# Kernel optimization log

Hardware: AMD Instinct MI355X
Metric: run time of the kernel (lower is better)

Reference implementation:

```python
import jax, jax.numpy as jnp
import numpy as np

B, N, C = 8, 4096, 768
H, HD = 12, 64          # num_heads, head_dim = C // H
M = HD * 2              # rand_feat_dim
LAM = 0.3
NUM_STEP = 5


def setup_inputs() -> dict:
    key = jax.random.key(0)
    k1, k2, k3, k4 = jax.random.split(key, 4)
    x = jax.random.normal(k1, (B, N, C), dtype=jnp.float32)
    Wqkv = jax.random.normal(k2, (C, 2 * C), dtype=jnp.float32) * 0.02
    Wproj = jax.random.normal(k3, (C, C), dtype=jnp.float32) * 0.02
    bproj = jnp.zeros((C,), dtype=jnp.float32)
    rand_matrix = jax.random.normal(k4, (H, HD, M), dtype=jnp.float32)
    return {"x": x, "Wqkv": Wqkv, "Wproj": Wproj, "bproj": bproj,
            "rand_matrix": rand_matrix}


def _soft(z, t):
    # sign(z) * relu(|z| - t): soft-thresholding (ISTA proximal step)
    return jnp.sign(z) * jax.nn.relu(jnp.abs(z) - t)


def reference(x, Wqkv, Wproj, bproj, rand_matrix):
    Bn, Nn, Cn = x.shape
    Hh, hd, m = rand_matrix.shape
    scale = hd ** (-0.5)

    qkv = x @ Wqkv                                   # [B,N,2C]
    q = qkv[..., :Cn].reshape(Bn, Nn, Hh, hd).transpose(0, 2, 1, 3)  # [B,H,N,hd]
    v = qkv[..., Cn:].reshape(Bn, Nn, Hh, hd).transpose(0, 2, 1, 3)  # [B,H,N,hd]

    # random-feature map: exp(q @ proj - ||q||^2 / 2) / sqrt(m)
    qs = q * scale ** 0.5
    rf = jnp.exp(jnp.einsum('bhnd,hdm->bhnm', qs, rand_matrix)
                 - 0.5 * jnp.sum(qs * qs, axis=-1, keepdims=True)) / m ** 0.5
    # F.normalize(p=2, dim=-2): normalize over the sequence axis
    qn = rf / jnp.maximum(jnp.linalg.norm(rf, axis=-2, keepdims=True), 1e-12)

    kk = jnp.einsum('bhnm,bhnp->bhmp', qn, qn)       # [B,H,m,m]
    kv = jnp.einsum('bhnm,bhnd->bhmd', qn, v)        # [B,H,m,hd]

    # Lipschitz bound: max row L1 norm of kk, detached
    L = jax.lax.stop_gradient(
        jnp.max(jnp.sum(jnp.abs(kk), axis=-1), axis=-1))[..., None, None] + 1.0

    # unrolled ISTA soft-thresholding loop
    s = _soft(kv, LAM)
    for _ in range(NUM_STEP):
        s = _soft(s - (kk @ s - kv) / L, LAM / L)

    out = jnp.einsum('bhnm,bhmd->bhnd', qn, s)       # [B,H,N,hd]
    out = out.transpose(0, 2, 1, 3).reshape(Bn, Nn, Cn)
    return out @ Wproj + bproj
```

## Files before the change

kernel.cpp:

```cpp
#include <hip/hip_runtime.h>


typedef __attribute__((ext_vector_type(8))) short bf16x8;
typedef __attribute__((ext_vector_type(4))) float f32x4;

#define GLD16(gptr, lptr)                                                              \
  __builtin_amdgcn_global_load_lds((const __attribute__((address_space(1))) void*)(gptr), \
                                   (__attribute__((address_space(3))) void*)(lptr), 16, 0, 0)

__device__ __forceinline__ unsigned short f2bf(float f) {
  union { float f; unsigned int u; } v; v.f = f;
  unsigned int r = v.u + 0x7fffu + ((v.u >> 16) & 1u);
  return (unsigned short)(r >> 16);
}
__device__ __forceinline__ float bf2f(unsigned short s) {
  union { unsigned int u; float f; } v; v.u = ((unsigned int)s) << 16;
  return v.f;
}
__device__ __forceinline__ float rn_of(float css) {
  return 1.f / fmaxf(sqrtf(css), 1e-12f);
}

template<int BM, int BN>
__device__ __forceinline__ void gemm_core_nt(
    const unsigned short* __restrict__ A, int lda,
    const unsigned short* __restrict__ B0,
    const unsigned short* __restrict__ B1, int brows0, int ldb,
    int K,
    f32x4 (&acc)[BM / 32][BN / 32],
    unsigned short* As, unsigned short* Bs) {
  constexpr int MT = BM / 32, NT = BN / 32;
  const int tid = threadIdx.x;
  const int lane = tid & 63, wave = tid >> 6;
  const int wm = (wave >> 1) * (BM / 2), wn = (wave & 1) * (BN / 2);
  const int l16 = lane & 15, quad = lane >> 4;
  const int arow = tid >> 2;
  const int akos = (((tid & 3) ^ ((arow >> 1) & 3)) << 3);
  const int fsw = (l16 >> 1) & 3;
#pragma unroll
  for (int i = 0; i < MT; i++)
#pragma unroll
    for (int j = 0; j < NT; j++)
#pragma unroll
      for (int r = 0; r < 4; r++) acc[i][j][r] = 0.f;

  for (int k0 = 0; k0 < K; k0 += 32) {
    __syncthreads();
#pragma unroll
    for (int c = 0; c < BM / 64; c++) {
      const unsigned short* gp = A + (long)(arow + c * 64) * lda + k0 + akos;
      GLD16(gp, As + (c * 256 + wave * 64) * 8);
    }
#pragma unroll
    for (int c = 0; c < BN / 64; c++) {
      int row = arow + c * 64;
      const unsigned short* bp = (row < brows0) ? (B0 + (long)row * ldb)
                                                : (B1 + (long)(row - brows0) * ldb);
      GLD16(bp + k0 + akos, Bs + (c * 256 + wave * 64) * 8);
    }
    __syncthreads();
    bf16x8 af[MT], bfr[NT];
#pragma unroll
    for (int i = 0; i < MT; i++)
      af[i] = *(const bf16x8*)(As + (wm + i * 16 + l16) * 32 + ((quad ^ fsw) * 8));
#pragma unroll
    for (int j = 0; j < NT; j++)
      bfr[j] = *(const bf16x8*)(Bs + (wn + j * 16 + l16) * 32 + ((quad ^ fsw) * 8));
#pragma unroll
    for (int i = 0; i < MT; i++)
#pragma unroll
      for (int j = 0; j < NT; j++)
        acc[i][j] = __builtin_amdgcn_mfma_f32_16x16x32_bf16(af[i], bfr[j], acc[i][j], 0, 0, 0);
  }
}

__global__ __launch_bounds__(256) void k_convert_bf16(const float* __restrict__ in,
                                                      unsigned short* __restrict__ out, long n4) {
  long i = (long)blockIdx.x * 256 + threadIdx.x;
  if (i < n4) {
    float4 v = ((const float4*)in)[i];
    unsigned short o[4] = {f2bf(v.x), f2bf(v.y), f2bf(v.z), f2bf(v.w)};
    ((uint2*)out)[i] = *(uint2*)o;
  }
}

__global__ __launch_bounds__(256) void k_transpose_tiled(const float* __restrict__ in,
                                                         unsigned short* __restrict__ out,
                                                         int R, int C, float scale) {
  __shared__ float t[32][33];
  const float* ib = in + (long)blockIdx.z * R * C;
  unsigned short* ob = out + (long)blockIdx.z * R * C;
  int c0 = blockIdx.x * 32, r0 = blockIdx.y * 32;
  int tx = threadIdx.x & 31, ty = threadIdx.x >> 5;
#pragma unroll
  for (int k = 0; k < 32; k += 8)
    t[ty + k][tx] = ib[(long)(r0 + ty + k) * C + c0 + tx];
  __syncthreads();
#pragma unroll
  for (int k = 0; k < 32; k += 8)
    ob[(long)(c0 + ty + k) * R + r0 + tx] = f2bf(t[tx][ty + k] * scale);
}

__global__ __launch_bounds__(256) void k_gemm_qkv(const unsigned short* __restrict__ xbf,
                                                  const unsigned short* __restrict__ wqkvT,
                                                  unsigned short* __restrict__ q,
                                                  unsigned short* __restrict__ vT) {
  __shared__ __align__(16) unsigned short pool[8576];
  unsigned short* As = pool;
  unsigned short* Bs = pool + 4096;
  f32x4 acc[4][4];
  const int L = blockIdx.x;
  const int xcd = L & 7, slot = L >> 3;
  const int rt = xcd * 32 + slot / 12;
  const int ct = slot % 12;
  const int tid = threadIdx.x, lane = tid & 63, wave = tid >> 6;
  const int l16 = lane & 15, quad = lane >> 4;
  const int wm = (wave >> 1) * 64, wn = (wave & 1) * 64;

  const unsigned short* A = xbf + (long)rt * 128 * 768;
  const unsigned short* B = wqkvT + (long)ct * 128 * 768;
  gemm_core_nt<128, 128>(A, 768, B, B, 128, 768, 768, acc, As, Bs);

  const int b = rt >> 5;
  const int nbase = (rt & 31) * 128;
  if (ct < 6) {
#pragma unroll
    for (int i = 0; i < 4; i++)
#pragma unroll
      for (int j = 0; j < 4; j++)
#pragma unroll
        for (int r = 0; r < 4; r++) {
          int col = ct * 128 + wn + j * 16 + l16;
          int h = col >> 6, d = col & 63;
          int n = nbase + wm + i * 16 + quad * 4 + r;
          q[((long)(b * 12 + h) * 4096 + n) * 64 + d] = f2bf(acc[i][j][r]);
        }
  } else {
    for (int hh = 0; hh < 2; hh++) {
      __syncthreads();
      if ((wave >> 1) == hh) {
#pragma unroll
        for (int i = 0; i < 4; i++)
#pragma unroll
          for (int j = 0; j < 4; j++)
#pragma unroll
            for (int r = 0; r < 4; r++)
              pool[(i * 16 + quad * 4 + r) * 134 + wn + j * 16 + l16] = f2bf(acc[i][j][r]);
      }
      __syncthreads();
#pragma unroll
      for (int c = 0; c < 4; c++) {
        int chunk = tid + c * 256;
        int col = chunk >> 3, nj = (chunk & 7) * 8;
        unsigned short o[8];
#pragma unroll
        for (int e = 0; e < 8; e++) o[e] = pool[(nj + e) * 134 + col];
        int vcol = ct * 128 - 768 + col;
        int h = vcol >> 6, d = vcol & 63;
        long n = nbase + hh * 64 + nj;
        *(uint4*)&vT[((long)(b * 12 + h) * 64 + d) * 4096 + n] = *(uint4*)o;
      }
    }
  }
}

__global__ __launch_bounds__(256) void k_gemm_rf(const unsigned short* __restrict__ q,
                                                 const unsigned short* __restrict__ rmT,
                                                 unsigned short* __restrict__ qnT,
                                                 float* __restrict__ colss) {
  __shared__ __align__(16) unsigned short smem[16384];
  __shared__ float hnp[256];
  __shared__ float css[128];
  unsigned short* Asm = smem;
  unsigned short* Bsm = smem + 8192;
  unsigned short* pool = smem;
  f32x4 acc[4][4];
  const int nt = blockIdx.x, bh = blockIdx.y, h = bh % 12;
  const int tid = threadIdx.x, lane = tid & 63, wave = tid >> 6;
  const int l16 = lane & 15, quad = lane >> 4;
  const int wm = (wave >> 1) * 64, wn = (wave & 1) * 64;
  const int fsw = (l16 >> 1) & 3;
  const unsigned short* Aq = q + ((long)bh * 4096 + nt * 128) * 64;
  const unsigned short* Brm = rmT + (long)h * 8192;

#pragma unroll
  for (int c = 0; c < 4; c++) {
    int chunk = c * 256 + tid;
    int row = chunk >> 3, ko8 = chunk & 7;
    int kc = ko8 >> 2;
    int c2s = (ko8 & 3) ^ ((row >> 1) & 3);
    *(uint4*)(Asm + kc * 4096 + row * 32 + c2s * 8) = *(const uint4*)(Aq + (long)row * 64 + ko8 * 8);
    *(uint4*)(Bsm + kc * 4096 + row * 32 + c2s * 8) = *(const uint4*)(Brm + (long)row * 64 + ko8 * 8);
  }
  for (int i = tid; i < 128; i += 256) css[i] = 0.f;
  __syncthreads();
  {
    const unsigned short* ap = Asm + (tid & 1) * 4096 + (tid >> 1) * 32;
    float ssum = 0.f;
#pragma unroll
    for (int e = 0; e < 32; e++) { float f = bf2f(ap[e]); ssum += f * f; }
    hnp[tid] = ssum;
  }
#pragma unroll
  for (int i = 0; i < 4; i++)
#pragma unroll
    for (int j = 0; j < 4; j++)
#pragma unroll
      for (int r = 0; r < 4; r++) acc[i][j][r] = 0.f;
#pragma unroll
  for (int kc = 0; kc < 2; kc++) {
    bf16x8 af[4], bfr[4];
#pragma unroll
    for (int i = 0; i < 4; i++)
      af[i] = *(const bf16x8*)(Asm + kc * 4096 + (wm + i * 16 + l16) * 32 + ((quad ^ fsw) * 8));
#pragma unroll
    for (int j = 0; j < 4; j++)
      bfr[j] = *(const bf16x8*)(Bsm + kc * 4096 + (wn + j * 16 + l16) * 32 + ((quad ^ fsw) * 8));
#pragma unroll
    for (int i = 0; i < 4; i++)
#pragma unroll
      for (int j = 0; j < 4; j++)
        acc[i][j] = __builtin_amdgcn_mfma_f32_16x16x32_bf16(af[i], bfr[j], acc[i][j], 0, 0, 0);
  }
  __syncthreads();
  float hnv[4][4];
#pragma unroll
  for (int i = 0; i < 4; i++)
#pragma unroll
    for (int r = 0; r < 4; r++) {
      int row = wm + i * 16 + quad * 4 + r;
      hnv[i][r] = 0.0625f * (hnp[2 * row] + hnp[2 * row + 1]);
    }
#pragma unroll
  for (int j = 0; j < 4; j++) {
    int col = wn + j * 16 + l16;
    float cp = 0.f;
#pragma unroll
    for (int i = 0; i < 4; i++)
#pragma unroll
      for (int r = 0; r < 4; r++) {
        float v = __expf(acc[i][j][r] - hnv[i][r]) * 0.08838834764831845f;
        acc[i][j][r] = v;
        cp += v * v;
      }
    atomicAdd(&css[col], cp);
  }
  __syncthreads();
  for (int i = tid; i < 128; i += 256) atomicAdd(&colss[bh * 128 + i], css[i]);
  for (int hh = 0; hh < 2; hh++) {
    __syncthreads();
    if ((wave >> 1) == hh) {
#pragma unroll
      for (int i = 0; i < 4; i++)
#pragma unroll
        for (int j = 0; j < 4; j++)
#pragma unroll
          for (int r = 0; r < 4; r++)
            pool[(i * 16 + quad * 4 + r) * 134 + wn + j * 16 + l16] = f2bf(acc[i][j][r]);
    }
    __syncthreads();
#pragma unroll
    for (int c = 0; c < 4; c++) {
      int chunk = tid + c * 256;
      int m = chunk >> 3, nj = (chunk & 7) * 8;
      unsigned short o[8];
#pragma unroll
      for (int e = 0; e < 8; e++) o[e] = pool[(nj + e) * 134 + m];
      *(uint4*)&qnT[((long)bh * 128 + m) * 4096 + nt * 128 + hh * 64 + nj] = *(uint4*)o;
    }
  }
}

__global__ __launch_bounds__(256) void k_gemm_kkkv(const unsigned short* __restrict__ qnT,
                                                   const unsigned short* __restrict__ vT,
                                                   const float* __restrict__ colss,
                                                   unsigned short* __restrict__ kkp) {
  __shared__ __align__(16) unsigned short As[128 * 32], Bs[192 * 32];
  f32x4 acc[4][6];
  const int ks = blockIdx.x, bh = blockIdx.y;
  const unsigned short* A = qnT + (long)bh * 128 * 4096 + ks * 512;
  const unsigned short* B1 = vT + (long)bh * 64 * 4096 + ks * 512;
  gemm_core_nt<128, 192>(A, 4096, A, B1, 128, 4096, 512, acc, As, Bs);
  const int lane = threadIdx.x & 63, wave = threadIdx.x >> 6;
  const int l16 = lane & 15, quad = lane >> 4;
  const int wm = (wave >> 1) * 64, wn = (wave & 1) * 96;
  unsigned short* dst = kkp + ((long)ks * 96 + bh) * 24576;
  float rnr[4][4];
#pragma unroll
  for (int i = 0; i < 4; i++)
#pragma unroll
    for (int r = 0; r < 4; r++)
      rnr[i][r] = rn_of(colss[bh * 128 + wm + i * 16 + quad * 4 + r]);
#pragma unroll
  for (int j = 0; j < 6; j++) {
    int col = wn + j * 16 + l16;
    float rnc = (col < 128) ? rn_of(colss[bh * 128 + col]) : 1.f;
#pragma unroll
    for (int i = 0; i < 4; i++)
#pragma unroll
      for (int r = 0; r < 4; r++) {
        int row = wm + i * 16 + quad * 4 + r;
        dst[row * 192 + col] = f2bf(acc[i][j][r] * rnr[i][r] * rnc);
      }
  }
}

__global__ __launch_bounds__(256) void k_ista(const unsigned short* __restrict__ kkp,
                                              const float* __restrict__ colss,
                                              unsigned short* __restrict__ sT) {
  __shared__ __align__(16) unsigned short kks[128 * 144];
  __shared__ __align__(16) unsigned short ssT[64 * 144];
  __shared__ float kvs[128 * 64];
  __shared__ float red[128];
  __shared__ float rns[128];
  const int tid = threadIdx.x, lane = tid & 63, wave = tid >> 6;
  const int l16 = lane & 15, quad = lane >> 4;
  const int wm = (wave >> 1) * 64, wn = (wave & 1) * 32;
  const int bh = blockIdx.x;
  const unsigned short* base = kkp + (long)bh * 24576;
  for (int idx = tid; idx < 3072; idx += 256) {
    int m = idx / 24, c8 = idx % 24;
    float f[8] = {0.f, 0.f, 0.f, 0.f, 0.f, 0.f, 0.f, 0.f};
#pragma unroll
    for (int ks = 0; ks < 8; ks++) {
      union { uint4 u; unsigned short s[8]; } u;
      u.u = *(const uint4*)(base + (long)ks * 2359296 + m * 192 + c8 * 8);
#pragma unroll
      for (int e = 0; e < 8; e++) f[e] += bf2f(u.s[e]);
    }
    if (c8 < 16) {
#pragma unroll
      for (int e = 0; e < 8; e++) kks[m * 144 + c8 * 8 + e] = f2bf(f[e]);
    } else {
#pragma unroll
      for (int e = 0; e < 8; e++) kvs[m * 64 + (c8 - 16) * 8 + e] = f[e];
    }
  }
  __syncthreads();
  float kv[4][2][4];
#pragma unroll
  for (int i = 0; i < 4; i++)
#pragma unroll
    for (int j = 0; j < 2; j++)
#pragma unroll
      for (int r = 0; r < 4; r++) {
        int m = wm + i * 16 + quad * 4 + r, d = wn + j * 16 + l16;
        kv[i][j][r] = kvs[m * 64 + d];
      }
  if (tid < 128) {
    float rs = 0.f;
    const unsigned short* rp = kks + tid * 144;
    for (int p = 0; p < 128; p++) rs += fabsf(bf2f(rp[p]));
    red[tid] = rs;
    rns[tid] = rn_of(colss[bh * 128 + tid]);
  }
  __syncthreads();
  for (int o = 64; o > 0; o >>= 1) {
    if (tid < o) red[tid] = fmaxf(red[tid], red[tid + o]);
    __syncthreads();
  }
  const float L = red[0] + 1.f;
  const float invL = 1.f / L;
  const float lamL = 0.3f * invL;
  float sreg[4][2][4];
#pragma unroll
  for (int i = 0; i < 4; i++)
#pragma unroll
    for (int j = 0; j < 2; j++)
#pragma unroll
      for (int r = 0; r < 4; r++) {
        float z = kv[i][j][r];
        float az = fabsf(z) - 0.3f;
        float s = az > 0.f ? copysignf(az, z) : 0.f;
        sreg[i][j][r] = s;
        ssT[(wn + j * 16 + l16) * 144 + wm + i * 16 + quad * 4 + r] = f2bf(s);
      }
  for (int step = 0; step < 5; step++) {
    __syncthreads();
    f32x4 acc[4][2];
#pragma unroll
    for (int i = 0; i < 4; i++)
#pragma unroll
      for (int j = 0; j < 2; j++)
#pragma unroll
        for (int r = 0; r < 4; r++) acc[i][j][r] = 0.f;
#pragma unroll
    for (int kc = 0; kc < 4; kc++) {
      bf16x8 af[4], bfj[2];
#pragma unroll
      for (int i = 0; i < 4; i++)
        af[i] = *(const bf16x8*)(kks + (wm + i * 16 + l16) * 144 + kc * 32 + quad * 8);
#pragma unroll
      for (int j = 0; j < 2; j++)
        bfj[j] = *(const bf16x8*)(ssT + (wn + j * 16 + l16) * 144 + kc * 32 + quad * 8);
#pragma unroll
      for (int i = 0; i < 4; i++)
#pragma unroll
        for (int j = 0; j < 2; j++)
          acc[i][j] = __builtin_amdgcn_mfma_f32_16x16x32_bf16(af[i], bfj[j], acc[i][j], 0, 0, 0);
    }
    __syncthreads();
#pragma unroll
    for (int i = 0; i < 4; i++)
#pragma unroll
      for (int j = 0; j < 2; j++)
#pragma unroll
        for (int r = 0; r < 4; r++) {
          float z = sreg[i][j][r] - (acc[i][j][r] - kv[i][j][r]) * invL;
          float az = fabsf(z) - lamL;
          float s = az > 0.f ? copysignf(az, z) : 0.f;
          sreg[i][j][r] = s;
          ssT[(wn + j * 16 + l16) * 144 + wm + i * 16 + quad * 4 + r] = f2bf(s);
        }
  }
#pragma unroll
  for (int i = 0; i < 4; i++)
#pragma unroll
    for (int j = 0; j < 2; j++)
#pragma unroll
      for (int r = 0; r < 4; r++) {
        int m = wm + i * 16 + quad * 4 + r, d = wn + j * 16 + l16;
        sT[(long)bh * 8192 + d * 128 + m] = f2bf(sreg[i][j][r] * rns[m]);
      }
}

__global__ __launch_bounds__(256) void k_gemm_attn(const unsigned short* __restrict__ qnT,
                                                   const unsigned short* __restrict__ sT,
                                                   unsigned short* __restrict__ attn) {
  __shared__ __align__(16) unsigned short As2[32 * 128];
  __shared__ __align__(16) unsigned short Bs[64 * 32];
  f32x4 acc[4][2];
  const int nt = blockIdx.x, bh = blockIdx.y;
  const int b = bh / 12, h = bh % 12;
  const int tid = threadIdx.x, lane = tid & 63, wave = tid >> 6;
  const int l16 = lane & 15, quad = lane >> 4;
  const int wm = (wave >> 1) * 64, wn = (wave & 1) * 32;
  const int fsw = (l16 >> 1) & 3;
#pragma unroll
  for (int i = 0; i < 4; i++)
#pragma unroll
    for (int j = 0; j < 2; j++)
#pragma unroll
      for (int r = 0; r < 4; r++) acc[i][j][r] = 0.f;
  for (int k0 = 0; k0 < 128; k0 += 32) {
    __syncthreads();
#pragma unroll
    for (int c = 0; c < 2; c++) {
      int chunk = tid + c * 256;
      int kr = chunk >> 4, n0 = (chunk & 15) * 8;
      const unsigned short* gp = qnT + ((long)bh * 128 + k0 + kr) * 4096 + nt * 128 + n0;
      GLD16(gp, As2 + (c * 256 + wave * 64) * 8);
    }
    {
      int dd = tid >> 2;
      int ko = (((tid & 3) ^ ((dd >> 1) & 3)) * 8);
      const unsigned short* gp = sT + ((long)bh * 64 + dd) * 128 + k0 + ko;
      GLD16(gp, Bs + wave * 512);
    }
    __syncthreads();
    bf16x8 af[4], bfr[2];
#pragma unroll
    for (int i = 0; i < 4; i++) {
      union { bf16x8 v; unsigned short s[8]; } u;
#pragma unroll
      for (int e = 0; e < 8; e++) u.s[e] = As2[(quad * 8 + e) * 128 + wm + i * 16 + l16];
      af[i] = u.v;
    }
#pragma unroll
    for (int j = 0; j < 2; j++)
      bfr[j] = *(const bf16x8*)&Bs[(wn + j * 16 + l16) * 32 + ((quad ^ fsw) * 8)];
#pragma unroll
    for (int i = 0; i < 4; i++)
#pragma unroll
      for (int j = 0; j < 2; j++)
        acc[i][j] = __builtin_amdgcn_mfma_f32_16x16x32_bf16(af[i], bfr[j], acc[i][j], 0, 0, 0);
  }
#pragma unroll
  for (int i = 0; i < 4; i++)
#pragma unroll
    for (int j = 0; j < 2; j++)
#pragma unroll
      for (int r = 0; r < 4; r++) {
        int n = nt * 128 + wm + i * 16 + quad * 4 + r;
        int dd = wn + j * 16 + l16;
        attn[((long)b * 4096 + n) * 768 + h * 64 + dd] = f2bf(acc[i][j][r]);
      }
}

__global__ __launch_bounds__(256) void k_gemm_proj(const unsigned short* __restrict__ attn,
                                                   const unsigned short* __restrict__ wprojT,
                                                   const float* __restrict__ bias,
                                                   float* __restrict__ out) {
  __shared__ __align__(16) unsigned short As[128 * 32], Bs[128 * 32];
  f32x4 acc[4][4];
  const int Lb = blockIdx.x;
  const int xcd = Lb & 7, slot = Lb >> 3;
  const int rt = xcd * 32 + slot / 6;
  const int ct = slot % 6;
  const unsigned short* A = attn + (long)rt * 128 * 768;
  const unsigned short* B = wprojT + (long)ct * 128 * 768;
  gemm_core_nt<128, 128>(A, 768, B, B, 128, 768, 768, acc, As, Bs);
  const int lane = threadIdx.x & 63, wave = threadIdx.x >> 6;
  const int l16 = lane & 15, quad = lane >> 4;
  const int wm = (wave >> 1) * 64, wn = (wave & 1) * 64;
  long row0 = (long)rt * 128, col0 = (long)ct * 128;
#pragma unroll
  for (int i = 0; i < 4; i++)
#pragma unroll
    for (int j = 0; j < 4; j++) {
      int col = (int)col0 + wn + j * 16 + l16;
      float bv = bias[col];
#pragma unroll
      for (int r = 0; r < 4; r++) {
        long row = row0 + wm + i * 16 + quad * 4 + r;
        out[row * 768 + col] = acc[i][j][r] + bv;
      }
    }
}

extern "C" void kernel_launch(void* const* d_in, const int* in_sizes, int n_in,
                              void* d_out, int out_size, void* d_ws, size_t ws_size,
                              hipStream_t stream) {
  const float* x = (const float*)d_in[0];
  const float* Wqkv = (const float*)d_in[1];
  const float* Wproj = (const float*)d_in[2];
  const float* bproj = (const float*)d_in[3];
  const float* rm = (const float*)d_in[4];
  float* out = (float*)d_out;

  size_t o = 0;
  char* wsb = (char*)d_ws;
  auto take = [&](size_t b) { char* p = wsb + o; o += b; return p; };
  unsigned short* wqkvT = (unsigned short*)take(2359296);
  unsigned short* wprojT = (unsigned short*)take(1179648);
  unsigned short* rmT = (unsigned short*)take(196608);
  unsigned short* q = (unsigned short*)take(50331648);
  unsigned short* vT = (unsigned short*)take(50331648);
  float* colss = (float*)take(49152);
  unsigned short* sT = (unsigned short*)take(1572864);
  if (ws_size < o) return;

  unsigned short* xbf = (unsigned short*)d_out;
  unsigned short* qnT = (unsigned short*)d_out;
  unsigned short* kkp = q;
  unsigned short* attnbf = q;

  hipMemsetAsync(colss, 0, 49152, stream);

  k_convert_bf16<<<24576, 256, 0, stream>>>(x, xbf, 6291456L);
  k_transpose_tiled<<<dim3(48, 24, 1), 256, 0, stream>>>(Wqkv, wqkvT, 768, 1536, 1.0f);
  k_transpose_tiled<<<dim3(24, 24, 1), 256, 0, stream>>>(Wproj, wprojT, 768, 768, 1.0f);
  k_transpose_tiled<<<dim3(4, 2, 12), 256, 0, stream>>>(rm, rmT, 64, 128, 0.3535533905932738f);
  k_gemm_qkv<<<3072, 256, 0, stream>>>(xbf, wqkvT, q, vT);
  k_gemm_rf<<<dim3(32, 96), 256, 0, stream>>>(q, rmT, qnT, colss);
  k_gemm_kkkv<<<dim3(8, 96), 256, 0, stream>>>(qnT, vT, colss, kkp);
  k_ista<<<96, 256, 0, stream>>>(kkp, colss, sT);
  k_gemm_attn<<<dim3(32, 96), 256, 0, stream>>>(qnT, sT, attnbf);
  k_gemm_proj<<<1536, 256, 0, stream>>>(attnbf, wprojT, bproj, out);
}
```

Measured before the change: 471.5 us.

## Use 256x256 tiled 8-wave GEMM core for QKV and projection GEMMs

Adds a new GEMM core with 256x256 block tiles, 512 threads, double-buffered direct-to-LDS loads, and MFMA work split into two halves around the prefetch, with priority hints. The QKV and output-projection GEMMs move to this core with larger tiles and fewer blocks, aiming for better operand reuse and overlap of loads with MFMA. The V transpose epilogue is rewritten to read contiguous LDS rows. The trade-off is more registers and LDS per block and fewer blocks, which lowers occupancy and can leave the tail poorly balanced.

```diff
diff --git a/kernel.cpp b/kernel.cpp
--- a/kernel.cpp
+++ b/kernel.cpp
@@ -19,6 +19,90 @@
 }
 __device__ __forceinline__ float rn_of(float css) {
   return 1.f / fmaxf(sqrtf(css), 1e-12f);
+}
+
+template<int KT>
+__device__ __forceinline__ void gemm256_core(
+    const unsigned short* __restrict__ A,
+    const unsigned short* __restrict__ B,
+    int ldk,
+    f32x4 (&acc)[8][4],
+    unsigned short* smem) {
+  const int tid = threadIdx.x;
+  const int lane = tid & 63, wave = tid >> 6;
+  const int l16 = lane & 15, quad = lane >> 4;
+  const int wr = wave >> 2, wc = wave & 3;
+  const int fsw = (l16 >> 1) & 3;
+  const int r0 = tid >> 2;
+  const int gsw = (((tid & 3) ^ ((r0 >> 1) & 3)) << 3);
+
+#pragma unroll
+  for (int i = 0; i < 8; i++)
+#pragma unroll
+    for (int j = 0; j < 4; j++)
+#pragma unroll
+      for (int r = 0; r < 4; r++) acc[i][j][r] = 0.f;
+
+  const unsigned short* Ag0 = A + (long)r0 * ldk + gsw;
+  const unsigned short* Ag1 = A + (long)(r0 + 128) * ldk + gsw;
+  const unsigned short* Bg0 = B + (long)r0 * ldk + gsw;
+  const unsigned short* Bg1 = B + (long)(r0 + 128) * ldk + gsw;
+  const int ldsW = wave * 64 * 8;
+
+  auto stage = [&](int t, int b) {
+    unsigned short* Ab = smem + b * 16384;
+    unsigned short* Bb = Ab + 8192;
+    const int k0 = t * 32;
+    GLD16(Ag0 + k0, Ab + ldsW);
+    GLD16(Ag1 + k0, Ab + 4096 + ldsW);
+    GLD16(Bg0 + k0, Bb + ldsW);
+    GLD16(Bg1 + k0, Bb + 4096 + ldsW);
+  };
+
+  stage(0, 0);
+  stage(1, 1);
+  asm volatile("s_waitcnt vmcnt(4)" ::: "memory");
+  __builtin_amdgcn_s_barrier();
+
+  for (int t = 0; t < KT; t++) {
+    const int b = t & 1;
+    const unsigned short* Ab = smem + b * 16384;
+    const unsigned short* Bb = Ab + 8192;
+    bf16x8 af[8], bf[4];
+#pragma unroll
+    for (int i = 0; i < 8; i++)
+      af[i] = *(const bf16x8*)(Ab + (wr * 128 + i * 16 + l16) * 32 + ((quad ^ fsw) * 8));
+#pragma unroll
+    for (int j = 0; j < 4; j++)
+      bf[j] = *(const bf16x8*)(Bb + (wc * 64 + j * 16 + l16) * 32 + ((quad ^ fsw) * 8));
+    asm volatile("s_waitcnt lgkmcnt(0)" ::: "memory");
+    __builtin_amdgcn_s_barrier();
+    __builtin_amdgcn_s_setprio(1);
+#pragma unroll
+    for (int i = 0; i < 8; i++)
+#pragma unroll
+      for (int j = 0; j < 2; j++)
+        acc[i][j] = __builtin_amdgcn_mfma_f32_16x16x32_bf16(af[i], bf[j], acc[i][j], 0, 0, 0);
+    __builtin_amdgcn_s_setprio(0);
+    asm volatile("" ::: "memory");
+    __builtin_amdgcn_s_barrier();
+    if (t + 2 < KT) stage(t + 2, b);
+    asm volatile("" ::: "memory");
+    __builtin_amdgcn_s_barrier();
+    __builtin_amdgcn_s_setprio(1);
+#pragma unroll
+    for (int i = 0; i < 8; i++)
+#pragma unroll
+      for (int j = 2; j < 4; j++)
+        acc[i][j] = __builtin_amdgcn_mfma_f32_16x16x32_bf16(af[i], bf[j], acc[i][j], 0, 0, 0);
+    __builtin_amdgcn_s_setprio(0);
+    if (t + 2 < KT) {
+      asm volatile("s_waitcnt vmcnt(4)" ::: "memory");
+    } else {
+      asm volatile("s_waitcnt vmcnt(0)" ::: "memory");
+    }
+    __builtin_amdgcn_s_barrier();
+  }
 }
 
 template<int BM, int BN>
@@ -101,64 +185,59 @@
     ob[(long)(c0 + ty + k) * R + r0 + tx] = f2bf(t[tx][ty + k] * scale);
 }
 
-__global__ __launch_bounds__(256) void k_gemm_qkv(const unsigned short* __restrict__ xbf,
-                                                  const unsigned short* __restrict__ wqkvT,
-                                                  unsigned short* __restrict__ q,
-                                                  unsigned short* __restrict__ vT) {
-  __shared__ __align__(16) unsigned short pool[8576];
-  unsigned short* As = pool;
-  unsigned short* Bs = pool + 4096;
-  f32x4 acc[4][4];
+__global__ __launch_bounds__(512, 2) void k_gemm_qkv256(const unsigned short* __restrict__ xbf,
+                                                        const unsigned short* __restrict__ wqkvT,
+                                                        unsigned short* __restrict__ q,
+                                                        unsigned short* __restrict__ vT) {
+  __shared__ __align__(16) unsigned short smem[36864];
+  f32x4 acc[8][4];
   const int L = blockIdx.x;
   const int xcd = L & 7, slot = L >> 3;
-  const int rt = xcd * 32 + slot / 12;
-  const int ct = slot % 12;
+  const int rt = xcd * 16 + slot / 6;
+  const int ct = slot % 6;
+  gemm256_core<24>(xbf + (long)rt * 256 * 768, wqkvT + (long)ct * 256 * 768, 768, acc, smem);
+
   const int tid = threadIdx.x, lane = tid & 63, wave = tid >> 6;
   const int l16 = lane & 15, quad = lane >> 4;
-  const int wm = (wave >> 1) * 64, wn = (wave & 1) * 64;
-
-  const unsigned short* A = xbf + (long)rt * 128 * 768;
-  const unsigned short* B = wqkvT + (long)ct * 128 * 768;
-  gemm_core_nt<128, 128>(A, 768, B, B, 128, 768, 768, acc, As, Bs);
-
-  const int b = rt >> 5;
-  const int nbase = (rt & 31) * 128;
-  if (ct < 6) {
-#pragma unroll
-    for (int i = 0; i < 4; i++)
-#pragma unroll
-      for (int j = 0; j < 4; j++)
+  const int wr = wave >> 2, wc = wave & 3;
+  const int b = rt >> 4;
+  const int nbase = (rt & 15) * 256;
+  if (ct < 3) {
+#pragma unroll
+    for (int i = 0; i < 8; i++)
+#pragma unroll
+      for (int j = 0; j < 4; j++) {
+        int col = ct * 256 + wc * 64 + j * 16 + l16;
+        int h = col >> 6, d = col & 63;
 #pragma unroll
         for (int r = 0; r < 4; r++) {
-          int col = ct * 128 + wn + j * 16 + l16;
-          int h = col >> 6, d = col & 63;
-          int n = nbase + wm + i * 16 + quad * 4 + r;
+          int n = nbase + wr * 128 + i * 16 + quad * 4 + r;
           q[((long)(b * 12 + h) * 4096 + n) * 64 + d] = f2bf(acc[i][j][r]);
         }
+      }
   } else {
+    unsigned short* pool = smem;
     for (int hh = 0; hh < 2; hh++) {
       __syncthreads();
-      if ((wave >> 1) == hh) {
-#pragma unroll
-        for (int i = 0; i < 4; i++)
+      if (wr == hh) {
+#pragma unroll
+        for (int i = 0; i < 8; i++)
 #pragma unroll
           for (int j = 0; j < 4; j++)
 #pragma unroll
             for (int r = 0; r < 4; r++)
-              pool[(i * 16 + quad * 4 + r) * 134 + wn + j * 16 + l16] = f2bf(acc[i][j][r]);
+              pool[(wc * 64 + j * 16 + l16) * 136 + i * 16 + quad * 4 + r] = f2bf(acc[i][j][r]);
       }
       __syncthreads();
 #pragma unroll
-      for (int c = 0; c < 4; c++) {
-        int chunk = tid + c * 256;
-        int col = chunk >> 3, nj = (chunk & 7) * 8;
-        unsigned short o[8];
-#pragma unroll
-        for (int e = 0; e < 8; e++) o[e] = pool[(nj + e) * 134 + col];
-        int vcol = ct * 128 - 768 + col;
+      for (int it = 0; it < 8; it++) {
+        int chunk = it * 512 + tid;
+        int col = chunk >> 4, ng = chunk & 15;
+        uint4 val = *(const uint4*)&pool[col * 136 + ng * 8];
+        int vcol = (ct - 3) * 256 + col;
         int h = vcol >> 6, d = vcol & 63;
-        long n = nbase + hh * 64 + nj;
-        *(uint4*)&vT[((long)(b * 12 + h) * 64 + d) * 4096 + n] = *(uint4*)o;
+        long n = nbase + hh * 128 + ng * 8;
+        *(uint4*)&vT[((long)(b * 12 + h) * 64 + d) * 4096 + n] = val;
       }
     }
   }
@@ -487,32 +566,30 @@
       }
 }
 
-__global__ __launch_bounds__(256) void k_gemm_proj(const unsigned short* __restrict__ attn,
-                                                   const unsigned short* __restrict__ wprojT,
-                                                   const float* __restrict__ bias,
-                                                   float* __restrict__ out) {
-  __shared__ __align__(16) unsigned short As[128 * 32], Bs[128 * 32];
-  f32x4 acc[4][4];
-  const int Lb = blockIdx.x;
-  const int xcd = Lb & 7, slot = Lb >> 3;
-  const int rt = xcd * 32 + slot / 6;
-  const int ct = slot % 6;
-  const unsigned short* A = attn + (long)rt * 128 * 768;
-  const unsigned short* B = wprojT + (long)ct * 128 * 768;
-  gemm_core_nt<128, 128>(A, 768, B, B, 128, 768, 768, acc, As, Bs);
-  const int lane = threadIdx.x & 63, wave = threadIdx.x >> 6;
-  const int l16 = lane & 15, quad = lane >> 4;
-  const int wm = (wave >> 1) * 64, wn = (wave & 1) * 64;
-  long row0 = (long)rt * 128, col0 = (long)ct * 128;
-#pragma unroll
-  for (int i = 0; i < 4; i++)
+__global__ __launch_bounds__(512, 2) void k_gemm_proj256(const unsigned short* __restrict__ attn,
+                                                         const unsigned short* __restrict__ wprojT,
+                                                         const float* __restrict__ bias,
+                                                         float* __restrict__ out) {
+  __shared__ __align__(16) unsigned short smem[32768];
+  f32x4 acc[8][4];
+  const int L = blockIdx.x;
+  const int xcd = L & 7, slot = L >> 3;
+  const int rt = xcd * 16 + slot / 3;
+  const int ct = slot % 3;
+  gemm256_core<24>(attn + (long)rt * 256 * 768, wprojT + (long)ct * 256 * 768, 768, acc, smem);
+  const int tid = threadIdx.x, lane = tid & 63, wave = tid >> 6;
+  const int l16 = lane & 15, quad = lane >> 4;
+  const int wr = wave >> 2, wc = wave & 3;
+  const long row0 = (long)rt * 256 + wr * 128;
+#pragma unroll
+  for (int i = 0; i < 8; i++)
 #pragma unroll
     for (int j = 0; j < 4; j++) {
-      int col = (int)col0 + wn + j * 16 + l16;
+      int col = ct * 256 + wc * 64 + j * 16 + l16;
       float bv = bias[col];
 #pragma unroll
       for (int r = 0; r < 4; r++) {
-        long row = row0 + wm + i * 16 + quad * 4 + r;
+        long row = row0 + i * 16 + quad * 4 + r;
         out[row * 768 + col] = acc[i][j][r] + bv;
       }
     }
@@ -551,10 +628,10 @@
   k_transpose_tiled<<<dim3(48, 24, 1), 256, 0, stream>>>(Wqkv, wqkvT, 768, 1536, 1.0f);
   k_transpose_tiled<<<dim3(24, 24, 1), 256, 0, stream>>>(Wproj, wprojT, 768, 768, 1.0f);
   k_transpose_tiled<<<dim3(4, 2, 12), 256, 0, stream>>>(rm, rmT, 64, 128, 0.3535533905932738f);
-  k_gemm_qkv<<<3072, 256, 0, stream>>>(xbf, wqkvT, q, vT);
+  k_gemm_qkv256<<<768, 512, 0, stream>>>(xbf, wqkvT, q, vT);
   k_gemm_rf<<<dim3(32, 96), 256, 0, stream>>>(q, rmT, qnT, colss);
   k_gemm_kkkv<<<dim3(8, 96), 256, 0, stream>>>(qnT, vT, colss, kkp);
   k_ista<<<96, 256, 0, stream>>>(kkp, colss, sT);
   k_gemm_attn<<<dim3(32, 96), 256, 0, stream>>>(qnT, sT, attnbf);
-  k_gemm_proj<<<1536, 256, 0, stream>>>(attnbf, wprojT, bproj, out);
-}
+  k_gemm_proj256<<<1536 / 4, 512, 0, stream>>>(attnbf, wprojT, bproj, out);
+}
```

Result: no change. 472.3 us (+0.2%).
